# Optimization experiments

Hardware: AMD Instinct MI355X
Metric: run time of the kernel (lower is better)

The kernel has to match this reference:

```python
import jax, jax.numpy as jnp
import numpy as np

B, T, D = 256, 64, 512          # batch, seq_len, enc_input_size == dec_output_size
HE, L = 1024, 512               # enc_hidden_size, latent == con_hidden == dec_hidden
BAR, BAR_UNITS = 4, 16          # conductor bars, steps per bar (BAR*BAR_UNITS == T)


def _lstm_step(x, h, c, Wih, Whh, bih, bhh):
    # torch LSTM gate order: i, f, g, o
    g = x @ Wih.T + bih + h @ Whh.T + bhh
    i, f, gg, o = jnp.split(g, 4, axis=-1)
    c = jax.nn.sigmoid(f) * c + jax.nn.sigmoid(i) * jnp.tanh(gg)
    h = jax.nn.sigmoid(o) * jnp.tanh(c)
    return h, c


def _run_lstm_final_h(x_t, Wih, Whh, bih, bhh):
    # x_t: (T, B, D_in); returns final hidden state (B, H)
    Bb = x_t.shape[1]
    H = Whh.shape[1]
    init = (jnp.zeros((Bb, H), x_t.dtype), jnp.zeros((Bb, H), x_t.dtype))
    def step(carry, xt):
        h, c = _lstm_step(xt, carry[0], carry[1], Wih, Whh, bih, bhh)
        return (h, c), None
    (h, _), _ = jax.lax.scan(step, init, x_t)
    return h


def reference(x, eps, We_ih_f, We_hh_f, be_ih_f, be_hh_f, We_ih_b, We_hh_b, be_ih_b, be_hh_b,
              Wmu, bmu, Wstd, bstd, Wc_ih0, Wc_hh0, bc_ih0, bc_hh0, Wc_ih1, Wc_hh1, bc_ih1, bc_hh1,
              Wcl, bcl, Wd_ih0, Wd_hh0, bd_ih0, bd_hh0, Wd_ih1, Wd_hh1, bd_ih1, bd_hh1, Wlog, blog):
    x_t = jnp.transpose(x, (1, 0, 2))  # (T, B, D)
    # ---- Encoder: 1-layer bidirectional LSTM, take final hidden of each direction ----
    h_f = _run_lstm_final_h(x_t, We_ih_f, We_hh_f, be_ih_f, be_hh_f)
    h_b = _run_lstm_final_h(x_t[::-1], We_ih_b, We_hh_b, be_ih_b, be_hh_b)
    henc = jnp.concatenate([h_f, h_b], axis=-1)  # (B, 2*HE)
    mu_raw = henc @ Wmu.T + bmu
    mu = (mu_raw - mu_raw.mean(-1, keepdims=True)) / jnp.sqrt(mu_raw.var(-1, keepdims=True) + 1e-5)
    std = jax.nn.softplus(henc @ Wstd.T + bstd)
    z = mu + eps * std  # (B, L)
    # ---- Conductor: 2-layer LSTM, h0=c0=z, input is z at every bar step ----
    h0 = c0 = h1 = c1 = z
    feats = []
    for _ in range(BAR):
        h0, c0 = _lstm_step(z, h0, c0, Wc_ih0, Wc_hh0, bc_ih0, bc_hh0)
        h1, c1 = _lstm_step(h0, h1, c1, Wc_ih1, Wc_hh1, bc_ih1, bc_hh1)
        feats.append(h1)
    feat = jnp.stack(feats, axis=1) @ Wcl.T + bcl  # (B, BAR, L)
    # ---- Decoder: 2-layer LSTM, teacher-forced, hidden reset to bar embedding each bar ----
    z_t = jnp.transpose(jnp.repeat(feat, BAR_UNITS, axis=1), (1, 0, 2))  # (T, B, L)
    x_prev_t = jnp.concatenate([jnp.zeros((1, x.shape[0], D), x.dtype), x_t[:-1]], axis=0)
    reset_t = (jnp.arange(T) % BAR_UNITS) == 0
    zH = jnp.zeros((x.shape[0], L), x.dtype)
    def dec_step(carry, inp):
        hd1, cd1, hd2, cd2 = carry
        xp, zb, rs = inp
        hd1 = jnp.where(rs, zb, hd1); cd1 = jnp.where(rs, zb, cd1)
        hd2 = jnp.where(rs, zb, hd2); cd2 = jnp.where(rs, zb, cd2)
        xin = jnp.concatenate([xp, zb], axis=-1)  # (B, D+L)
        hd1, cd1 = _lstm_step(xin, hd1, cd1, Wd_ih0, Wd_hh0, bd_ih0, bd_hh0)
        hd2, cd2 = _lstm_step(hd1, hd2, cd2, Wd_ih1, Wd_hh1, bd_ih1, bd_hh1)
        logits = hd2 @ Wlog.T + blog  # temp == 1
        return (hd1, cd1, hd2, cd2), logits
    _, logits_t = jax.lax.scan(dec_step, (zH, zH, zH, zH), (x_prev_t, z_t, reset_t))
    prob = jnp.transpose(jax.nn.softmax(logits_t, axis=-1), (1, 0, 2))  # (B, T, D)
    label = jnp.argmax(prob, axis=-1).astype(jnp.float32)  # (B, T)
    return prob, mu, std, label


def setup_inputs() -> dict:
    key = jax.random.key(0)
    ks = iter(jax.random.split(key, 40))
    def w(shape, fan):
        return jax.random.normal(next(ks), shape, jnp.float32) * (1.0 / np.sqrt(fan))
    return {
        'x': jax.random.normal(next(ks), (B, T, D), jnp.float32),
        'eps': jax.random.normal(next(ks), (B, L), jnp.float32),
        'We_ih_f': w((4 * HE, D), HE), 'We_hh_f': w((4 * HE, HE), HE),
        'be_ih_f': w((4 * HE,), HE), 'be_hh_f': w((4 * HE,), HE),
        'We_ih_b': w((4 * HE, D), HE), 'We_hh_b': w((4 * HE, HE), HE),
        'be_ih_b': w((4 * HE,), HE), 'be_hh_b': w((4 * HE,), HE),
        'Wmu': w((L, 2 * HE), 2 * HE), 'bmu': w((L,), 2 * HE),
        'Wstd': w((L, 2 * HE), 2 * HE), 'bstd': w((L,), 2 * HE),
        'Wc_ih0': w((4 * L, L), L), 'Wc_hh0': w((4 * L, L), L),
        'bc_ih0': w((4 * L,), L), 'bc_hh0': w((4 * L,), L),
        'Wc_ih1': w((4 * L, L), L), 'Wc_hh1': w((4 * L, L), L),
        'bc_ih1': w((4 * L,), L), 'bc_hh1': w((4 * L,), L),
        'Wcl': w((L, L), L), 'bcl': w((L,), L),
        'Wd_ih0': w((4 * L, L + D), L), 'Wd_hh0': w((4 * L, L), L),
        'bd_ih0': w((4 * L,), L), 'bd_hh0': w((4 * L,), L),
        'Wd_ih1': w((4 * L, L), L), 'Wd_hh1': w((4 * L, L), L),
        'bd_ih1': w((4 * L,), L), 'bd_hh1': w((4 * L,), L),
        'Wlog': w((D, L), L), 'blog': w((D,), L),
    }
```

## Files before the change

kernel.cpp:

```cpp
#include <hip/hip_runtime.h>
#include <cstddef>
#include <cstdint>

static constexpr int B  = 256;
static constexpr int T  = 64;
static constexpr int D  = 512;
static constexpr int HE = 1024;
static constexpr int L  = 512;

typedef unsigned short ushort_t;
typedef __attribute__((ext_vector_type(8))) short short8;
typedef __attribute__((ext_vector_type(8))) unsigned short ushort8_t;
typedef __attribute__((ext_vector_type(8))) _Float16 f16x8;
typedef __attribute__((ext_vector_type(4))) float f32x4;
typedef __attribute__((ext_vector_type(4))) unsigned short ushort4_t;

static constexpr float LO_SCALE   = 2048.0f;
static constexpr float LO_UNSCALE = 4.8828125e-4f;

__device__ __forceinline__ float sigmoidf_(float x) { return 1.0f / (1.0f + expf(-x)); }

struct hfp { ushort_t hi, lo; };
__device__ __forceinline__ hfp f16_split(float v) {
    _Float16 h = (_Float16)v;
    _Float16 l = (_Float16)((v - (float)h) * LO_SCALE);
    hfp r;
    r.hi = __builtin_bit_cast(ushort_t, h);
    r.lo = __builtin_bit_cast(ushort_t, l);
    return r;
}

__device__ __forceinline__ size_t tile_off(int m, int n, int ldt) {
    return ((size_t)(m >> 4) * ldt + (n >> 5)) * 512
         + (size_t)((((m & 15) + (((n >> 3) & 3) << 4)) << 3) + (n & 7));
}

struct PkSeg { const float* src; ushort_t* hi; ushort_t* lo; int K, H, base; };
struct PkAll { PkSeg s[16]; int total; };

__global__ void pack_all(PkAll pa)
{
    int idx = blockIdx.x * 256 + threadIdx.x;
    if (idx >= pa.total) return;
    int si = 0;
#pragma unroll
    for (int i = 1; i < 16; ++i) if (idx >= pa.s[i].base) si = i;
    const PkSeg sg = pa.s[si];
    int c = idx - sg.base;
    int ldt = sg.K >> 5;
    int t = c >> 6;
    int lane = c & 63;
    int m15 = lane & 15;
    int kg  = lane >> 4;
    int p  = (t / ldt) * 16 + m15;
    int k0 = (t % ldt) * 32 + kg * 8;
    int srow = p;
    if (sg.H) srow = ((p >> 4) & 3) * sg.H + (p >> 6) * 16 + (p & 15);
    const float* s = sg.src + (size_t)srow * sg.K + k0;
    ushort8_t h, l;
#pragma unroll
    for (int j = 0; j < 8; ++j) {
        hfp a = f16_split(s[j]);
        h[j] = a.hi; l[j] = a.lo;
    }
    size_t off = (size_t)t * 512 + lane * 8;
    *(ushort8_t*)(sg.hi + off) = h;
    *(ushort8_t*)(sg.lo + off) = l;
}

struct PbSeg { const float* b1; const float* b2; float* dst; int H, base; };
struct PbAll { PbSeg s[6]; int total; };

__global__ void pack_bias_all(PbAll pb)
{
    int idx = blockIdx.x * 256 + threadIdx.x;
    if (idx >= pb.total) return;
    int si = 0;
#pragma unroll
    for (int i = 1; i < 6; ++i) if (idx >= pb.s[i].base) si = i;
    const PbSeg sg = pb.s[si];
    int p = idx - sg.base;
    int srow = ((p >> 4) & 3) * sg.H + (p >> 6) * 16 + (p & 15);
    sg.dst[p] = sg.b1[srow] + sg.b2[srow];
}

__global__ void conv_x(const float* __restrict__ x, ushort_t* __restrict__ xh,
                       ushort_t* __restrict__ xl)
{
    int idx = blockIdx.x * 256 + threadIdx.x;
    if (idx >= T * B * D / 8) return;
    int slab = idx >> 14;
    int c2 = idx & 16383;
    int t2 = c2 >> 6;
    int lane = c2 & 63;
    int tr = t2 >> 4, tc = t2 & 15;
    int b  = tr * 16 + (lane & 15);
    int k0 = tc * 32 + (lane >> 4) * 8;
    const float* s = x + ((size_t)b * T + slab) * D + k0;
    ushort8_t h, l;
#pragma unroll
    for (int j = 0; j < 8; ++j) {
        hfp a = f16_split(s[j]);
        h[j] = a.hi; l[j] = a.lo;
    }
    size_t off = (size_t)slab * B * D + (size_t)t2 * 512 + lane * 8;
    *(ushort8_t*)(xh + off) = h;
    *(ushort8_t*)(xl + off) = l;
}

struct Op {
    const ushort_t *Ahi, *Alo; int ldtA, kt0A;
    const ushort_t *Whi, *Wlo; int ldtW, kt0W;
    int K;
};
struct MArgs {
    Op op[3];
    const float* ci0; int ld0;
    int mode;
    const float* cin; int cinLd;
    float* cout; int coutLd;
    ushort_t *hHi, *hLo; int hLdT;
    float* out; int outLd;
    ushort_t *pHi, *pLo; int pLdT;
};

__device__ __forceinline__ f32x4 MFH(short8 a, short8 w, f32x4 c) {
    return __builtin_amdgcn_mfma_f32_16x16x32_f16(
        __builtin_bit_cast(f16x8, a), __builtin_bit_cast(f16x8, w), c, 0, 0, 0);
}

template<int TAG, int WIDE>
__global__ __launch_bounds__(256) void gemm_sk(MArgs ga0, MArgs ga1)
{
    __shared__ float LV[4][2][4][4][64];
    const MArgs& ga = blockIdx.z ? ga1 : ga0;
    const int tid  = threadIdx.x;
    const int lane = tid & 63;
    const int wk   = tid >> 6;
    const int bid = blockIdx.x;
    int bx, by, m_w;
    if (WIDE) {
        bx = ((bid >> 5) << 3) | (bid & 7);
        by = (bid >> 3) & 3;
        m_w = (blockIdx.y * 4 + by) * 64;
    } else {
        bx = ((bid >> 6) << 3) | (bid & 7);
        by = (bid >> 3) & 7;
        m_w = (blockIdx.y * 8 + by) * 32;
    }
    const int n_w = bx * 64;
    const int l15 = lane & 15;
    const int mbase = (m_w >> 4) + (WIDE ? (wk & 1) * 2 : 0);

    f32x4 accH[2][4], accL[2][4];
#pragma unroll
    for (int mf = 0; mf < 2; ++mf)
#pragma unroll
        for (int j = 0; j < 4; ++j)
#pragma unroll
            for (int r = 0; r < 4; ++r) { accH[mf][j][r] = 0.0f; accL[mf][j][r] = 0.0f; }

    int NT = 0;
#pragma unroll
    for (int opi = 0; opi < 3; ++opi)
        if (ga.op[opi].Ahi && ga.op[opi].K > 0) NT += ga.op[opi].K >> 5;
    const int share = WIDE ? (NT >> 1) : (NT >> 2);
    int skip = (WIDE ? (wk >> 1) : wk) * share, cnt = share;

#pragma unroll 1
    for (int opi = 0; opi < 3 && cnt > 0; ++opi) {
        const Op o = ga.op[opi];
        if (o.Ahi == nullptr || o.K <= 0) continue;
        const int NK = o.K >> 5;
        if (skip >= NK) { skip -= NK; continue; }
        const int k0 = skip;
        const int k1 = (NK - k0 < cnt) ? NK : k0 + cnt;
        cnt -= (k1 - k0);
        skip = 0;

        const ushort_t *aHp[2], *aLp[2], *wHp[4], *wLp[4];
#pragma unroll
        for (int mf = 0; mf < 2; ++mf) {
            size_t ro = ((size_t)(mbase + mf) * o.ldtA + o.kt0A) * 512 + lane * 8;
            aHp[mf] = o.Ahi + ro; aLp[mf] = o.Alo + ro;
        }
#pragma unroll
        for (int j = 0; j < 4; ++j) {
            size_t ro = ((size_t)((n_w >> 4) + j) * o.ldtW + o.kt0W) * 512 + lane * 8;
            wHp[j] = o.Whi + ro; wLp[j] = o.Wlo + ro;
        }

        short8 A0[2], L0[2], W0[4], V0[4];
        short8 A1[2], L1[2], W1[4], V1[4];
        auto LD0 = [&](int ks) {
#pragma unroll
            for (int mf = 0; mf < 2; ++mf) {
                A0[mf] = *(const short8*)(aHp[mf] + (size_t)ks * 512);
                L0[mf] = *(const short8*)(aLp[mf] + (size_t)ks * 512);
            }
#pragma unroll
            for (int j = 0; j < 4; ++j) {
                W0[j] = *(const short8*)(wHp[j] + (size_t)ks * 512);
                V0[j] = *(const short8*)(wLp[j] + (size_t)ks * 512);
            }
        };
        auto LD1 = [&](int ks) {
#pragma unroll
            for (int mf = 0; mf < 2; ++mf) {
                A1[mf] = *(const short8*)(aHp[mf] + (size_t)ks * 512);
                L1[mf] = *(const short8*)(aLp[mf] + (size_t)ks * 512);
            }
#pragma unroll
            for (int j = 0; j < 4; ++j) {
                W1[j] = *(const short8*)(wHp[j] + (size_t)ks * 512);
                V1[j] = *(const short8*)(wLp[j] + (size_t)ks * 512);
            }
        };
        auto MM0 = [&]() {
#pragma unroll
            for (int mf = 0; mf < 2; ++mf)
#pragma unroll
                for (int j = 0; j < 4; ++j) {
                    accL[mf][j] = MFH(A0[mf], V0[j], accL[mf][j]);
                    accL[mf][j] = MFH(L0[mf], W0[j], accL[mf][j]);
                    accH[mf][j] = MFH(A0[mf], W0[j], accH[mf][j]);
                }
        };
        auto MM1 = [&]() {
#pragma unroll
            for (int mf = 0; mf < 2; ++mf)
#pragma unroll
                for (int j = 0; j < 4; ++j) {
                    accL[mf][j] = MFH(A1[mf], V1[j], accL[mf][j]);
                    accL[mf][j] = MFH(L1[mf], W1[j], accL[mf][j]);
                    accH[mf][j] = MFH(A1[mf], W1[j], accH[mf][j]);
                }
        };

        LD0(k0);
        int ks = k0;
        for (; ks + 2 < k1; ks += 2) {
            LD1(ks + 1);
            MM0();
            LD0(ks + 2);
            MM1();
        }
        if (ks + 1 < k1) { LD1(ks + 1); MM0(); MM1(); }
        else MM0();
    }

#pragma unroll
    for (int mf = 0; mf < 2; ++mf)
#pragma unroll
        for (int j = 0; j < 4; ++j)
#pragma unroll
            for (int r = 0; r < 4; ++r)
                LV[wk][mf][j][r][lane] = accH[mf][j][r] + LO_UNSCALE * accL[mf][j][r];
    __syncthreads();

    if (WIDE) {
        const int lt = wk;
        const int wb = lt >> 1;
        const int mfl = lt & 1;
#pragma unroll
        for (int r = 0; r < 4; ++r) {
            float g[4];
#pragma unroll
            for (int j = 0; j < 4; ++j) {
                float s = LV[wb][mfl][j][r][lane] + LV[wb + 2][mfl][j][r][lane];
                if (ga.ci0) s += ga.ci0[n_w + j * 16 + l15];
                g[j] = s;
            }
            const int m = m_w + lt * 16 + (lane >> 4) * 4 + r;
            if (ga.mode == 1) {
                const int n = (n_w >> 6) * 16 + l15;
                const float cold = ga.cin[(size_t)m * ga.cinLd + n];
                const float cn = sigmoidf_(g[1]) * cold + sigmoidf_(g[0]) * tanhf(g[2]);
                const float h  = sigmoidf_(g[3]) * tanhf(cn);
                ga.cout[(size_t)m * ga.coutLd + n] = cn;
                hfp hp = f16_split(h);
                size_t off = tile_off(m, n, ga.hLdT);
                ga.hHi[off] = hp.hi;
                ga.hLo[off] = hp.lo;
            } else {
#pragma unroll
                for (int j = 0; j < 4; ++j) {
                    const int p = n_w + j * 16 + l15;
                    int dst = m;
                    if (ga.mode == 2) dst = ((m & (B - 1)) << 6) + (m >> 8);
                    if (ga.out) ga.out[(size_t)dst * ga.outLd + p] = g[j];
                    if (ga.pHi) {
                        hfp vp = f16_split(g[j]);
                        size_t off = tile_off(m, p, ga.pLdT);
                        ga.pHi[off] = vp.hi;
                        ga.pLo[off] = vp.lo;
                    }
                }
            }
        }
    } else {
        const int mf = wk >> 1;
        const int rb = (wk & 1) * 2;
#pragma unroll
        for (int rr = 0; rr < 2; ++rr) {
            const int r = rb + rr;
            float g[4];
#pragma unroll
            for (int j = 0; j < 4; ++j) {
                float s = 0.0f;
#pragma unroll
                for (int w2 = 0; w2 < 4; ++w2) s += LV[w2][mf][j][r][lane];
                if (ga.ci0) s += ga.ci0[n_w + j * 16 + l15];
                g[j] = s;
            }
            const int m = m_w + mf * 16 + (lane >> 4) * 4 + r;
            if (ga.mode == 1) {
                const int n = (n_w >> 6) * 16 + l15;
                const float cold = ga.cin[(size_t)m * ga.cinLd + n];
                const float cn = sigmoidf_(g[1]) * cold + sigmoidf_(g[0]) * tanhf(g[2]);
                const float h  = sigmoidf_(g[3]) * tanhf(cn);
                ga.cout[(size_t)m * ga.coutLd + n] = cn;
                hfp hp = f16_split(h);
                size_t off = tile_off(m, n, ga.hLdT);
                ga.hHi[off] = hp.hi;
                ga.hLo[off] = hp.lo;
            } else {
#pragma unroll
                for (int j = 0; j < 4; ++j) {
                    const int p = n_w + j * 16 + l15;
                    int dst = m;
                    if (ga.mode == 2) dst = ((m & (B - 1)) << 6) + (m >> 8);
                    if (ga.out) ga.out[(size_t)dst * ga.outLd + p] = g[j];
                    if (ga.pHi) {
                        hfp vp = f16_split(g[j]);
                        size_t off = tile_off(m, p, ga.pLdT);
                        ga.pHi[off] = vp.hi;
                        ga.pLo[off] = vp.lo;
                    }
                }
            }
        }
    }
}

template<int TAG, int MF, int WM, int WN>
__global__ __launch_bounds__(WM * WN * 64) void gemm_t(MArgs ga0, MArgs ga1)
{
    const MArgs& ga = blockIdx.z ? ga1 : ga0;
    const int lane = threadIdx.x & 63;
    const int wid  = threadIdx.x >> 6;
    const int wy = wid / WN, wx = wid % WN;
    const int m_w = blockIdx.y * (WM * MF * 16) + wy * MF * 16;
    const int n_w = blockIdx.x * (WN * 64) + wx * 64;
    const int l15 = lane & 15;
    const int rB  = (lane >> 4) * 4;

    f32x4 accH[MF][4];
    f32x4 accL[MF][4];
#pragma unroll
    for (int mf = 0; mf < MF; ++mf)
#pragma unroll
        for (int j = 0; j < 4; ++j) {
            const int p = n_w + j * 16 + l15;
#pragma unroll
            for (int r = 0; r < 4; ++r) {
                float v = 0.0f;
                if (ga.ci0) v += ga.ci0[(size_t)(m_w + mf * 16 + rB + r) * ga.ld0 + p];
                accH[mf][j][r] = v;
                accL[mf][j][r] = 0.0f;
            }
        }

#pragma unroll 1
    for (int opi = 0; opi < 3; ++opi) {
        const Op o = ga.op[opi];
        if (o.Ahi == nullptr || o.K <= 0) continue;
        const ushort_t *aH[MF], *aL[MF], *wH[4], *wL[4];
#pragma unroll
        for (int mf = 0; mf < MF; ++mf) {
            size_t ro = ((size_t)((m_w >> 4) + mf) * o.ldtA + o.kt0A) * 512 + lane * 8;
            aH[mf] = o.Ahi + ro; aL[mf] = o.Alo + ro;
        }
#pragma unroll
        for (int j = 0; j < 4; ++j) {
            size_t ro = ((size_t)((n_w >> 4) + j) * o.ldtW + o.kt0W) * 512 + lane * 8;
            wH[j] = o.Whi + ro; wL[j] = o.Wlo + ro;
        }
        const int NK = o.K >> 5;

        auto LD = [&](short8* ah, short8* al, short8* wh, short8* wl, int ks) {
#pragma unroll
            for (int mf = 0; mf < MF; ++mf) {
                ah[mf] = *(const short8*)(aH[mf] + (size_t)ks * 512);
                al[mf] = *(const short8*)(aL[mf] + (size_t)ks * 512);
            }
#pragma unroll
            for (int j = 0; j < 4; ++j) {
                wh[j] = *(const short8*)(wH[j] + (size_t)ks * 512);
                wl[j] = *(const short8*)(wL[j] + (size_t)ks * 512);
            }
        };
        auto MM = [&](short8* ah, short8* al, short8* wh, short8* wl) {
#pragma unroll
            for (int mf = 0; mf < MF; ++mf)
#pragma unroll
                for (int j = 0; j < 4; ++j) {
                    accL[mf][j] = MFH(ah[mf], wl[j], accL[mf][j]);
                    accL[mf][j] = MFH(al[mf], wh[j], accL[mf][j]);
                    accH[mf][j] = MFH(ah[mf], wh[j], accH[mf][j]);
                }
        };

        short8 A0[MF], L0[MF], W0[4], V0[4];
        short8 A1[MF], L1[MF], W1[4], V1[4];
        LD(A0, L0, W0, V0, 0);
        int ks = 0;
        for (; ks + 2 < NK; ks += 2) {
            LD(A1, L1, W1, V1, ks + 1);
            MM(A0, L0, W0, V0);
            LD(A0, L0, W0, V0, ks + 2);
            MM(A1, L1, W1, V1);
        }
        LD(A1, L1, W1, V1, ks + 1);
        MM(A0, L0, W0, V0);
        MM(A1, L1, W1, V1);
    }

    if (ga.mode == 1) {
        const int n = (n_w >> 6) * 16 + l15;
#pragma unroll
        for (int mf = 0; mf < MF; ++mf)
#pragma unroll
            for (int r = 0; r < 4; ++r) {
                const int m = m_w + mf * 16 + rB + r;
                const float gi = accH[mf][0][r] + LO_UNSCALE * accL[mf][0][r];
                const float gf = accH[mf][1][r] + LO_UNSCALE * accL[mf][1][r];
                const float gg = accH[mf][2][r] + LO_UNSCALE * accL[mf][2][r];
                const float go = accH[mf][3][r] + LO_UNSCALE * accL[mf][3][r];
                const float cold = ga.cin[(size_t)m * ga.cinLd + n];
                const float cn = sigmoidf_(gf) * cold + sigmoidf_(gi) * tanhf(gg);
                const float h  = sigmoidf_(go) * tanhf(cn);
                ga.cout[(size_t)m * ga.coutLd + n] = cn;
                hfp hp = f16_split(h);
                size_t off = tile_off(m, n, ga.hLdT);
                ga.hHi[off] = hp.hi;
                ga.hLo[off] = hp.lo;
            }
    } else {
#pragma unroll
        for (int mf = 0; mf < MF; ++mf)
#pragma unroll
            for (int j = 0; j < 4; ++j) {
                const int p = n_w + j * 16 + l15;
#pragma unroll
                for (int r = 0; r < 4; ++r) {
                    const int m = m_w + mf * 16 + rB + r;
                    const float v = accH[mf][j][r] + LO_UNSCALE * accL[mf][j][r];
                    int dst = m;
                    if (ga.mode == 2) dst = ((m & (B - 1)) << 6) + (m >> 8);
                    if (ga.out) ga.out[(size_t)dst * ga.outLd + p] = v;
                    if (ga.pHi) {
                        hfp vp = f16_split(v);
                        size_t off = tile_off(m, p, ga.pLdT);
                        ga.pHi[off] = vp.hi;
                        ga.pLo[off] = vp.lo;
                    }
                }
            }
    }
}

__global__ void latent2(float* __restrict__ mu, float* __restrict__ sd,
                        const float* __restrict__ eps, float* __restrict__ c0,
                        float* __restrict__ c1, ushort_t* __restrict__ zh,
                        ushort_t* __restrict__ zl)
{
    const int b = blockIdx.x, l = threadIdx.x;
    float* mrow = mu + (size_t)b * L;
    float4 v0 = *(const float4*)(mrow + l * 4);
    float4 v1 = *(const float4*)(mrow + 256 + l * 4);
    float s = v0.x + v0.y + v0.z + v0.w + v1.x + v1.y + v1.z + v1.w;
    float q = v0.x * v0.x + v0.y * v0.y + v0.z * v0.z + v0.w * v0.w
            + v1.x * v1.x + v1.y * v1.y + v1.z * v1.z + v1.w * v1.w;
#pragma unroll
    for (int off = 32; off; off >>= 1) { s += __shfl_xor(s, off); q += __shfl_xor(q, off); }
    const float mean = s * (1.0f / 512.0f);
    const float var  = q * (1.0f / 512.0f) - mean * mean;
    const float inv  = rsqrtf(var + 1e-5f);
    v0.x = (v0.x - mean) * inv; v0.y = (v0.y - mean) * inv; v0.z = (v0.z - mean) * inv; v0.w = (v0.w - mean) * inv;
    v1.x = (v1.x - mean) * inv; v1.y = (v1.y - mean) * inv; v1.z = (v1.z - mean) * inv; v1.w = (v1.w - mean) * inv;
    *(float4*)(mrow + l * 4) = v0;
    *(float4*)(mrow + 256 + l * 4) = v1;

    float* srow = sd + (size_t)b * L;
    float4 s0 = *(const float4*)(srow + l * 4);
    float4 s1 = *(const float4*)(srow + 256 + l * 4);
    s0.x = fmaxf(s0.x, 0.0f) + log1pf(expf(-fabsf(s0.x)));
    s0.y = fmaxf(s0.y, 0.0f) + log1pf(expf(-fabsf(s0.y)));
    s0.z = fmaxf(s0.z, 0.0f) + log1pf(expf(-fabsf(s0.z)));
    s0.w = fmaxf(s0.w, 0.0f) + log1pf(expf(-fabsf(s0.w)));
    s1.x = fmaxf(s1.x, 0.0f) + log1pf(expf(-fabsf(s1.x)));
    s1.y = fmaxf(s1.y, 0.0f) + log1pf(expf(-fabsf(s1.y)));
    s1.z = fmaxf(s1.z, 0.0f) + log1pf(expf(-fabsf(s1.z)));
    s1.w = fmaxf(s1.w, 0.0f) + log1pf(expf(-fabsf(s1.w)));
    *(float4*)(srow + l * 4) = s0;
    *(float4*)(srow + 256 + l * 4) = s1;

    const float* erow = eps + (size_t)b * L;
    float4 e0 = *(const float4*)(erow + l * 4);
    float4 e1 = *(const float4*)(erow + 256 + l * 4);
    float4 z0, z1;
    z0.x = v0.x + e0.x * s0.x; z0.y = v0.y + e0.y * s0.y; z0.z = v0.z + e0.z * s0.z; z0.w = v0.w + e0.w * s0.w;
    z1.x = v1.x + e1.x * s1.x; z1.y = v1.y + e1.y * s1.y; z1.z = v1.z + e1.z * s1.z; z1.w = v1.w + e1.w * s1.w;
    *(float4*)(c0 + (size_t)b * L + l * 4) = z0;
    *(float4*)(c0 + (size_t)b * L + 256 + l * 4) = z1;
    *(float4*)(c1 + (size_t)b * L + l * 4) = z0;
    *(float4*)(c1 + (size_t)b * L + 256 + l * 4) = z1;
    ushort4_t h, lo;
    hfp a;
    a = f16_split(z0.x); h[0] = a.hi; lo[0] = a.lo;
    a = f16_split(z0.y); h[1] = a.hi; lo[1] = a.lo;
    a = f16_split(z0.z); h[2] = a.hi; lo[2] = a.lo;
    a = f16_split(z0.w); h[3] = a.hi; lo[3] = a.lo;
    size_t o0 = tile_off(b, l * 4, 16);
    *(ushort4_t*)(zh + o0) = h;
    *(ushort4_t*)(zl + o0) = lo;
    a = f16_split(z1.x); h[0] = a.hi; lo[0] = a.lo;
    a = f16_split(z1.y); h[1] = a.hi; lo[1] = a.lo;
    a = f16_split(z1.z); h[2] = a.hi; lo[2] = a.lo;
    a = f16_split(z1.w); h[3] = a.hi; lo[3] = a.lo;
    size_t o1 = tile_off(b, 256 + l * 4, 16);
    *(ushort4_t*)(zh + o1) = h;
    *(ushort4_t*)(zl + o1) = lo;
}

__global__ void softmax_all(float* __restrict__ prob, float* __restrict__ label)
{
    const int r = blockIdx.x, l = threadIdx.x;
    float* row = prob + (size_t)r * D;
    float4 x0 = *(const float4*)(row + l * 4);
    float4 x1 = *(const float4*)(row + 256 + l * 4);
    float m = x0.x; int mi = l * 4;
    { float v; int i;
      v = x0.y; i = l * 4 + 1;       if (v > m) { m = v; mi = i; }
      v = x0.z; i = l * 4 + 2;       if (v > m) { m = v; mi = i; }
      v = x0.w; i = l * 4 + 3;       if (v > m) { m = v; mi = i; }
      v = x1.x; i = 256 + l * 4;     if (v > m) { m = v; mi = i; }
      v = x1.y; i = 256 + l * 4 + 1; if (v > m) { m = v; mi = i; }
      v = x1.z; i = 256 + l * 4 + 2; if (v > m) { m = v; mi = i; }
      v = x1.w; i = 256 + l * 4 + 3; if (v > m) { m = v; mi = i; } }
#pragma unroll
    for (int off = 32; off; off >>= 1) {
        float om = __shfl_xor(m, off);
        int   oi = __shfl_xor(mi, off);
        if (om > m || (om == m && oi < mi)) { m = om; mi = oi; }
    }
    float4 e0, e1;
    e0.x = expf(x0.x - m); e0.y = expf(x0.y - m); e0.z = expf(x0.z - m); e0.w = expf(x0.w - m);
    e1.x = expf(x1.x - m); e1.y = expf(x1.y - m); e1.z = expf(x1.z - m); e1.w = expf(x1.w - m);
    float s = e0.x + e0.y + e0.z + e0.w + e1.x + e1.y + e1.z + e1.w;
#pragma unroll
    for (int off = 32; off; off >>= 1) s += __shfl_xor(s, off);
    const float inv = 1.0f / s;
    e0.x *= inv; e0.y *= inv; e0.z *= inv; e0.w *= inv;
    e1.x *= inv; e1.y *= inv; e1.z *= inv; e1.w *= inv;
    *(float4*)(row + l * 4) = e0;
    *(float4*)(row + 256 + l * 4) = e1;
    if (l == 0) label[r] = (float)mi;
}

extern "C" void kernel_launch(void* const* d_in, const int* in_sizes, int n_in,
                              void* d_out, int out_size, void* d_ws, size_t ws_size,
                              hipStream_t stream)
{
    const float* x       = (const float*)d_in[0];
    const float* eps     = (const float*)d_in[1];
    const float* We_ih_f = (const float*)d_in[2];
    const float* We_hh_f = (const float*)d_in[3];
    const float* be_ih_f = (const float*)d_in[4];
    const float* be_hh_f = (const float*)d_in[5];
    const float* We_ih_b = (const float*)d_in[6];
    const float* We_hh_b = (const float*)d_in[7];
    const float* be_ih_b = (const float*)d_in[8];
    const float* be_hh_b = (const float*)d_in[9];
    const float* Wmu     = (const float*)d_in[10];
    const float* bmu     = (const float*)d_in[11];
    const float* Wstd    = (const float*)d_in[12];
    const float* bstd    = (const float*)d_in[13];
    const float* Wc_ih0  = (const float*)d_in[14];
    const float* Wc_hh0  = (const float*)d_in[15];
    const float* bc_ih0  = (const float*)d_in[16];
    const float* bc_hh0  = (const float*)d_in[17];
    const float* Wc_ih1  = (const float*)d_in[18];
    const float* Wc_hh1  = (const float*)d_in[19];
    const float* bc_ih1  = (const float*)d_in[20];
    const float* bc_hh1  = (const float*)d_in[21];
    const float* Wcl     = (const float*)d_in[22];
    const float* bcl     = (const float*)d_in[23];
    const float* Wd_ih0  = (const float*)d_in[24];
    const float* Wd_hh0  = (const float*)d_in[25];
    const float* bd_ih0  = (const float*)d_in[26];
    const float* bd_hh0  = (const float*)d_in[27];
    const float* Wd_ih1  = (const float*)d_in[28];
    const float* Wd_hh1  = (const float*)d_in[29];
    const float* bd_ih1  = (const float*)d_in[30];
    const float* bd_hh1  = (const float*)d_in[31];
    const float* Wlog    = (const float*)d_in[32];
    const float* blog    = (const float*)d_in[33];
    (void)in_sizes; (void)n_in; (void)out_size;

    float* out      = (float*)d_out;
    float* prob_out = out;
    float* mu_out   = out + (size_t)B * T * D;
    float* std_out  = mu_out + (size_t)B * L;
    float* lab_out  = std_out + (size_t)B * L;

    char* cur = (char*)d_ws;
    auto alignup = [&]() { cur = (char*)(((uintptr_t)cur + 255) & ~(uintptr_t)255); };
    auto aU = [&](size_t elems) { alignup(); ushort_t* p = (ushort_t*)cur; cur += elems * 2; return p; };
    auto aF = [&](size_t elems) { alignup(); float* p = (float*)cur; cur += elems * 4; return p; };

    ushort_t* WefIh = aU((size_t)4*HE*D);  ushort_t* WefIl = aU((size_t)4*HE*D);
    ushort_t* WefHh = aU((size_t)4*HE*HE); ushort_t* WefHl = aU((size_t)4*HE*HE);
    ushort_t* WebIh = aU((size_t)4*HE*D);  ushort_t* WebIl = aU((size_t)4*HE*D);
    ushort_t* WebHh = aU((size_t)4*HE*HE); ushort_t* WebHl = aU((size_t)4*HE*HE);
    ushort_t* Wc0Ih = aU((size_t)4*L*L);   ushort_t* Wc0Il = aU((size_t)4*L*L);
    ushort_t* Wc0Hh = aU((size_t)4*L*L);   ushort_t* Wc0Hl = aU((size_t)4*L*L);
    ushort_t* Wc1Ih = aU((size_t)4*L*L);   ushort_t* Wc1Il = aU((size_t)4*L*L);
    ushort_t* Wc1Hh = aU((size_t)4*L*L);   ushort_t* Wc1Hl = aU((size_t)4*L*L);
    ushort_t* Wd0Ih = aU((size_t)4*L*(D+L)); ushort_t* Wd0Il = aU((size_t)4*L*(D+L));
    ushort_t* Wd0Hh = aU((size_t)4*L*L);   ushort_t* Wd0Hl = aU((size_t)4*L*L);
    ushort_t* Wd1Ih = aU((size_t)4*L*L);   ushort_t* Wd1Il = aU((size_t)4*L*L);
    ushort_t* Wd1Hh = aU((size_t)4*L*L);   ushort_t* Wd1Hl = aU((size_t)4*L*L);
    ushort_t* WmuH  = aU((size_t)L*2*HE);  ushort_t* WmuL  = aU((size_t)L*2*HE);
    ushort_t* WstdH = aU((size_t)L*2*HE);  ushort_t* WstdL = aU((size_t)L*2*HE);
    ushort_t* WclH  = aU((size_t)L*L);     ushort_t* WclL  = aU((size_t)L*L);
    ushort_t* WlogH = aU((size_t)D*L);     ushort_t* WlogL = aU((size_t)D*L);
    ushort_t* xh = aU((size_t)T*B*D);      ushort_t* xl = aU((size_t)T*B*D);
    ushort_t* hfh[2] = { aU((size_t)B*HE), aU((size_t)B*HE) };
    ushort_t* hfl[2] = { aU((size_t)B*HE), aU((size_t)B*HE) };
    ushort_t* hbh[2] = { aU((size_t)B*HE), aU((size_t)B*HE) };
    ushort_t* hbl[2] = { aU((size_t)B*HE), aU((size_t)B*HE) };
    ushort_t* zh = aU((size_t)B*L);        ushort_t* zl = aU((size_t)B*L);
    ushort_t* h0h[2] = { aU((size_t)B*L), aU((size_t)B*L) };
    ushort_t* h0l[2] = { aU((size_t)B*L), aU((size_t)B*L) };
    ushort_t* ftsH = aU((size_t)4*B*L);    ushort_t* ftsL = aU((size_t)4*B*L);
    ushort_t* featH = aU((size_t)4*B*L);   ushort_t* featL = aU((size_t)4*B*L);
    ushort_t* hd1h[2] = { aU((size_t)B*L), aU((size_t)B*L) };
    ushort_t* hd1l[2] = { aU((size_t)B*L), aU((size_t)B*L) };
    ushort_t* slabH = aU((size_t)T*B*L);   ushort_t* slabL = aU((size_t)T*B*L);
    float* cf   = aF((size_t)B*HE);
    float* cb   = aF((size_t)B*HE);
    float* zbuf = aF((size_t)B*HE);
    float* c0   = aF((size_t)B*L);
    float* c1   = aF((size_t)B*L);
    float* cd1  = aF((size_t)B*L);
    float* cd2  = aF((size_t)B*L);
    float* featF = aF((size_t)4*B*L);
    float* bEF = aF((size_t)4*HE);
    float* bEB = aF((size_t)4*HE);
    float* bC0 = aF((size_t)4*L);
    float* bC1 = aF((size_t)4*L);
    float* bD0 = aF((size_t)4*L);
    float* bD1 = aF((size_t)4*L);
    const size_t need = (size_t)(cur - (char*)d_ws);
    if (need > ws_size) return;

    {
        PkAll pa{};
        int base = 0, i = 0;
        auto add = [&](const float* s, ushort_t* h, ushort_t* l, int Np, int K, int H) {
            pa.s[i++] = { s, h, l, K, H, base };
            base += Np * (K >> 3);
        };
        add(We_ih_f, WefIh, WefIl, 4*HE, D, HE);
        add(We_hh_f, WefHh, WefHl, 4*HE, HE, HE);
        add(We_ih_b, WebIh, WebIl, 4*HE, D, HE);
        add(We_hh_b, WebHh, WebHl, 4*HE, HE, HE);
        add(Wc_ih0, Wc0Ih, Wc0Il, 4*L, L, L);
        add(Wc_hh0, Wc0Hh, Wc0Hl, 4*L, L, L);
        add(Wc_ih1, Wc1Ih, Wc1Il, 4*L, L, L);
        add(Wc_hh1, Wc1Hh, Wc1Hl, 4*L, L, L);
        add(Wd_ih0, Wd0Ih, Wd0Il, 4*L, D+L, L);
        add(Wd_hh0, Wd0Hh, Wd0Hl, 4*L, L, L);
        add(Wd_ih1, Wd1Ih, Wd1Il, 4*L, L, L);
        add(Wd_hh1, Wd1Hh, Wd1Hl, 4*L, L, L);
        add(Wmu,  WmuH,  WmuL,  L, 2*HE, 0);
        add(Wstd, WstdH, WstdL, L, 2*HE, 0);
        add(Wcl,  WclH,  WclL,  L, L, 0);
        add(Wlog, WlogH, WlogL, D, L, 0);
        pa.total = base;
        pack_all<<<(pa.total + 255) / 256, 256, 0, stream>>>(pa);

        PbAll pb{};
        int bb = 0, k = 0;
        auto addb = [&](const float* b1, const float* b2, float* dst, int H) {
            pb.s[k++] = { b1, b2, dst, H, bb };
            bb += 4 * H;
        };
        addb(be_ih_f, be_hh_f, bEF, HE);
        addb(be_ih_b, be_hh_b, bEB, HE);
        addb(bc_ih0, bc_hh0, bC0, L);
        addb(bc_ih1, bc_hh1, bC1, L);
        addb(bd_ih0, bd_hh0, bD0, L);
        addb(bd_ih1, bd_hh1, bD1, L);
        pb.total = bb;
        pack_bias_all<<<(pb.total + 255) / 256, 256, 0, stream>>>(pb);
    }
    conv_x<<<(T*B*D/8 + 255) / 256, 256, 0, stream>>>(x, xh, xl);
    (void)hipMemsetAsync(zbuf, 0, (size_t)B * HE * sizeof(float), stream);

    for (int t = 0; t < T; ++t) {
        MArgs f{};
        f.op[0] = { xh + (size_t)t*B*D, xl + (size_t)t*B*D, 16, 0, WefIh, WefIl, 16, 0, D };
        if (t) f.op[1] = { hfh[t&1], hfl[t&1], 32, 0, WefHh, WefHl, 32, 0, HE };
        f.ci0 = bEF; f.ld0 = 0;
        f.mode = 1;
        f.cin = t ? cf : zbuf; f.cinLd = HE;
        f.cout = cf; f.coutLd = HE;
        f.hHi = hfh[(t+1)&1]; f.hLo = hfl[(t+1)&1]; f.hLdT = 32;
        MArgs b = f;
        b.op[0] = { xh + (size_t)(T-1-t)*B*D, xl + (size_t)(T-1-t)*B*D, 16, 0, WebIh, WebIl, 16, 0, D };
        if (t) b.op[1] = { hbh[t&1], hbl[t&1], 32, 0, WebHh, WebHl, 32, 0, HE };
        b.ci0 = bEB;
        b.cin = t ? cb : zbuf;
        b.cout = cb;
        b.hHi = hbh[(t+1)&1]; b.hLo = hbl[(t+1)&1];
        gemm_sk<0,1><<<dim3((4*HE/64) * (B/64), 1, 2), 256, 0, stream>>>(f, b);
    }

    {
        MArgs m{};
        m.op[0] = { hfh[0], hfl[0], 32, 0, WmuH, WmuL, 64, 0, HE };
        m.op[1] = { hbh[0], hbl[0], 32, 0, WmuH, WmuL, 64, 32, HE };
        m.ci0 = bmu; m.ld0 = 0; m.mode = 0; m.out = mu_out; m.outLd = L;
        MArgs s = m;
        s.op[0].Whi = WstdH; s.op[0].Wlo = WstdL;
        s.op[1].Whi = WstdH; s.op[1].Wlo = WstdL;
        s.ci0 = bstd; s.out = std_out;
        gemm_sk<3,0><<<dim3((L/64) * (B/32), 1, 2), 256, 0, stream>>>(m, s);
        latent2<<<B, 64, 0, stream>>>(mu_out, std_out, eps, c0, c1, zh, zl);
    }

    auto condL1 = [&](int bar) {
        MArgs a{};
        a.op[0] = { zh, zl, 16, 0, Wc0Ih, Wc0Il, 16, 0, L };
        a.op[1] = { bar ? h0h[(bar-1)&1] : zh, bar ? h0l[(bar-1)&1] : zl, 16, 0, Wc0Hh, Wc0Hl, 16, 0, L };
        a.ci0 = bC0; a.ld0 = 0; a.mode = 1;
        a.cin = c0; a.cinLd = L; a.cout = c0; a.coutLd = L;
        a.hHi = h0h[bar&1]; a.hLo = h0l[bar&1]; a.hLdT = 16;
        return a;
    };
    auto condL2 = [&](int bar) {
        MArgs a2{};
        a2.op[0] = { h0h[bar&1], h0l[bar&1], 16, 0, Wc1Ih, Wc1Il, 16, 0, L };
        if (bar) a2.op[1] = { ftsH + (size_t)(bar-1)*B*L, ftsL + (size_t)(bar-1)*B*L, 16, 0, Wc1Hh, Wc1Hl, 16, 0, L };
        else     a2.op[1] = { zh, zl, 16, 0, Wc1Hh, Wc1Hl, 16, 0, L };
        a2.ci0 = bC1; a2.ld0 = 0; a2.mode = 1;
        a2.cin = c1; a2.cinLd = L; a2.cout = c1; a2.coutLd = L;
        a2.hHi = ftsH + (size_t)bar*B*L; a2.hLo = ftsL + (size_t)bar*B*L; a2.hLdT = 16;
        return a2;
    };
    {
        MArgs l1 = condL1(0);
        gemm_sk<2,0><<<dim3((4*L/64) * (B/32), 1, 1), 256, 0, stream>>>(l1, l1);
        for (int bar = 0; bar < 4; ++bar) {
            MArgs l2 = condL2(bar);
            if (bar + 1 < 4) {
                MArgs n1 = condL1(bar + 1);
                gemm_sk<2,0><<<dim3((4*L/64) * (B/32), 1, 2), 256, 0, stream>>>(l2, n1);
            } else {
                gemm_sk<2,0><<<dim3((4*L/64) * (B/32), 1, 1), 256, 0, stream>>>(l2, l2);
            }
        }
    }
    {
        MArgs af{};
        af.op[0] = { ftsH, ftsL, 16, 0, WclH, WclL, 16, 0, L };
        af.ci0 = bcl; af.ld0 = 0; af.mode = 0;
        af.out = featF; af.outLd = L;
        af.pHi = featH; af.pLo = featL; af.pLdT = 16;
        gemm_sk<5,0><<<dim3((L/64) * 8, 4*B/256, 1), 256, 0, stream>>>(af, af);
    }

    auto decG1 = [&](int t) {
        const int bar = t >> 4;
        const bool rs = (t & 15) == 0;
        MArgs g1{};
        if (t) g1.op[0] = { xh + (size_t)(t-1)*B*D, xl + (size_t)(t-1)*B*D, 16, 0, Wd0Ih, Wd0Il, 32, 0, D };
        g1.op[1] = { featH + (size_t)bar*B*L, featL + (size_t)bar*B*L, 16, 0, Wd0Ih, Wd0Il, 32, 16, L };
        if (rs) g1.op[2] = { featH + (size_t)bar*B*L, featL + (size_t)bar*B*L, 16, 0, Wd0Hh, Wd0Hl, 16, 0, L };
        else    g1.op[2] = { hd1h[(t-1)&1], hd1l[(t-1)&1], 16, 0, Wd0Hh, Wd0Hl, 16, 0, L };
        g1.ci0 = bD0; g1.ld0 = 0; g1.mode = 1;
        g1.cin = rs ? featF + (size_t)bar*B*L : cd1; g1.cinLd = L;
        g1.cout = cd1; g1.coutLd = L;
        g1.hHi = hd1h[t&1]; g1.hLo = hd1l[t&1]; g1.hLdT = 16;
        return g1;
    };
    auto decG2 = [&](int t) {
        const int bar = t >> 4;
        const bool rs = (t & 15) == 0;
        MArgs g2{};
        g2.op[0] = { hd1h[t&1], hd1l[t&1], 16, 0, Wd1Ih, Wd1Il, 16, 0, L };
        if (rs) g2.op[1] = { featH + (size_t)bar*B*L, featL + (size_t)bar*B*L, 16, 0, Wd1Hh, Wd1Hl, 16, 0, L };
        else    g2.op[1] = { slabH + (size_t)(t-1)*B*L, slabL + (size_t)(t-1)*B*L, 16, 0, Wd1Hh, Wd1Hl, 16, 0, L };
        g2.ci0 = bD1; g2.ld0 = 0; g2.mode = 1;
        g2.cin = rs ? featF + (size_t)bar*B*L : cd2; g2.cinLd = L;
        g2.cout = cd2; g2.coutLd = L;
        g2.hHi = slabH + (size_t)t*B*L; g2.hLo = slabL + (size_t)t*B*L; g2.hLdT = 16;
        return g2;
    };
    {
        MArgs g1 = decG1(0);
        gemm_sk<4,0><<<dim3((4*L/64) * (B/32), 1, 1), 256, 0, stream>>>(g1, g1);
        for (int t = 0; t < T; ++t) {
            MArgs g2 = decG2(t);
            if (t + 1 < T) {
                MArgs n1 = decG1(t + 1);
                gemm_sk<4,0><<<dim3((4*L/64) * (B/32), 1, 2), 256, 0, stream>>>(g2, n1);
            } else {
                gemm_sk<4,0><<<dim3((4*L/64) * (B/32), 1, 1), 256, 0, stream>>>(g2, g2);
            }
        }
    }

    {
        MArgs lg{};
        lg.op[0] = { slabH, slabL, 16, 0, WlogH, WlogL, 16, 0, L };
        lg.ci0 = blog; lg.ld0 = 0; lg.mode = 2;
        lg.out = prob_out; lg.outLd = D;
        gemm_t<5,2,2,4><<<dim3(D/256, T*B/64, 1), 512, 0, stream>>>(lg, lg);
    }
    softmax_all<<<B * T, 64, 0, stream>>>(prob_out, lab_out);
}
```

Baseline: 3.265 ms.

## Split encoder LSTM GEMM K-loop across eight waves per block

Adds a WIDE==2 variant of the split-K GEMM that launches 512 threads per block, giving four K-slices per output tile instead of two. The encoder recurrent step now uses this variant. Partial sums from the four slices are reduced through a larger shared-memory buffer, and the LSTM cell epilogue is spread across all eight waves. The aim is more latency hiding and parallelism on the serial, latency-bound timestep loop, at the cost of more shared-memory traffic and a larger reduction.

```diff
diff --git a/kernel.cpp b/kernel.cpp
--- a/kernel.cpp
+++ b/kernel.cpp
@@ -130,9 +130,9 @@
 }
 
 template<int TAG, int WIDE>
-__global__ __launch_bounds__(256) void gemm_sk(MArgs ga0, MArgs ga1)
+__global__ __launch_bounds__((WIDE == 2) ? 512 : 256) void gemm_sk(MArgs ga0, MArgs ga1)
 {
-    __shared__ float LV[4][2][4][4][64];
+    __shared__ float LV[(WIDE == 2) ? 8 : 4][2][4][4][64];
     const MArgs& ga = blockIdx.z ? ga1 : ga0;
     const int tid  = threadIdx.x;
     const int lane = tid & 63;
@@ -164,8 +164,8 @@
 #pragma unroll
     for (int opi = 0; opi < 3; ++opi)
         if (ga.op[opi].Ahi && ga.op[opi].K > 0) NT += ga.op[opi].K >> 5;
-    const int share = WIDE ? (NT >> 1) : (NT >> 2);
-    int skip = (WIDE ? (wk >> 1) : wk) * share, cnt = share;
+    const int share = (WIDE == 1) ? (NT >> 1) : (NT >> 2);
+    int skip = ((WIDE == 0) ? wk : (wk >> 1)) * share, cnt = share;
 
 #pragma unroll 1
     for (int opi = 0; opi < 3 && cnt > 0; ++opi) {
@@ -258,7 +258,50 @@
                 LV[wk][mf][j][r][lane] = accH[mf][j][r] + LO_UNSCALE * accL[mf][j][r];
     __syncthreads();
 
-    if (WIDE) {
+    if (WIDE == 2) {
+        const int lt = wk >> 1;
+        const int rb = (wk & 1) * 2;
+        const int gp = lt >> 1;
+        const int mfl = lt & 1;
+#pragma unroll
+        for (int rr = 0; rr < 2; ++rr) {
+            const int r = rb + rr;
+            float g[4];
+#pragma unroll
+            for (int j = 0; j < 4; ++j) {
+                float s = LV[gp][mfl][j][r][lane] + LV[gp + 2][mfl][j][r][lane]
+                        + LV[gp + 4][mfl][j][r][lane] + LV[gp + 6][mfl][j][r][lane];
+                if (ga.ci0) s += ga.ci0[n_w + j * 16 + l15];
+                g[j] = s;
+            }
+            const int m = m_w + lt * 16 + (lane >> 4) * 4 + r;
+            if (ga.mode == 1) {
+                const int n = (n_w >> 6) * 16 + l15;
+                const float cold = ga.cin[(size_t)m * ga.cinLd + n];
+                const float cn = sigmoidf_(g[1]) * cold + sigmoidf_(g[0]) * tanhf(g[2]);
+                const float h  = sigmoidf_(g[3]) * tanhf(cn);
+                ga.cout[(size_t)m * ga.coutLd + n] = cn;
+                hfp hp = f16_split(h);
+                size_t off = tile_off(m, n, ga.hLdT);
+                ga.hHi[off] = hp.hi;
+                ga.hLo[off] = hp.lo;
+            } else {
+#pragma unroll
+                for (int j = 0; j < 4; ++j) {
+                    const int p = n_w + j * 16 + l15;
+                    int dst = m;
+                    if (ga.mode == 2) dst = ((m & (B - 1)) << 6) + (m >> 8);
+                    if (ga.out) ga.out[(size_t)dst * ga.outLd + p] = g[j];
+                    if (ga.pHi) {
+                        hfp vp = f16_split(g[j]);
+                        size_t off = tile_off(m, p, ga.pLdT);
+                        ga.pHi[off] = vp.hi;
+                        ga.pLo[off] = vp.lo;
+                    }
+                }
+            }
+        }
+    } else if (WIDE == 1) {
         const int lt = wk;
         const int wb = lt >> 1;
         const int mfl = lt & 1;
@@ -726,7 +769,7 @@
         b.cin = t ? cb : zbuf;
         b.cout = cb;
         b.hHi = hbh[(t+1)&1]; b.hLo = hbl[(t+1)&1];
-        gemm_sk<0,1><<<dim3((4*HE/64) * (B/64), 1, 2), 256, 0, stream>>>(f, b);
+        gemm_sk<0,2><<<dim3((4*HE/64) * (B/64), 1, 2), 512, 0, stream>>>(f, b);
     }
 
     {
```

After: 3.381 ms. 1.04x slower.
